# Kernel optimization log

Hardware: AMD Instinct MI355X
Metric: run time of the kernel (lower is better)

Reference implementation:

```python
import jax, jax.numpy as jnp
import numpy as np

EPS = 1e-5
NEG_SLOPE = 0.2


def batchnorm_nodes(x, gamma, beta):
    # BatchNorm2d over channel=node axis; x: [N, T, D], stats over (T, D) per node
    m = x.mean(axis=(1, 2), keepdims=True)
    v = ((x - m) ** 2).mean(axis=(1, 2), keepdims=True)
    return (x - m) * jax.lax.rsqrt(v + EPS) * gamma[:, None, None] + beta[:, None, None]


def gat_relation(h, src, dst, W, al, ar, N):
    # h: [N, T, D]; W: [D, H, dh]; al/ar: [H, dh]
    z = jnp.einsum('ntd,dhe->nthe', h, W)              # [N, T, H, dh]
    el = jnp.einsum('nthe,he->nth', z, al)             # [N, T, H]
    er = jnp.einsum('nthe,he->nth', z, ar)
    e = jax.nn.leaky_relu(el[src] + er[dst], NEG_SLOPE)  # [E, T, H]
    emax = jax.ops.segment_max(e, dst, num_segments=N)   # [N, T, H]
    ex = jnp.exp(e - emax[dst])
    denom = jax.ops.segment_sum(ex, dst, num_segments=N)
    alpha = ex / jnp.maximum(denom[dst], 1e-16)          # segment softmax over in-edges
    msg = alpha[..., None] * z[src]                      # [E, T, H, dh]
    return jax.ops.segment_sum(msg, dst, num_segments=N)  # [N, T, H, dh]


def setup_inputs() -> dict:
    key = jax.random.key(0)
    ks = jax.random.split(key, 12)
    N, T, D, H, E, DFF = 10000, 12, 64, 4, 100000, 128
    dh = D // H
    s = 0.1
    return {
        'x': jax.random.normal(ks[0], (N, T, D), jnp.float32),
        'src1': jax.random.randint(ks[1], (E,), 0, N, jnp.int32),
        'dst1': jax.random.randint(ks[2], (E,), 0, N, jnp.int32),
        'src2': jax.random.randint(ks[3], (E,), 0, N, jnp.int32),
        'dst2': jax.random.randint(ks[4], (E,), 0, N, jnp.int32),
        'W1': jax.random.normal(ks[5], (D, H, dh), jnp.float32) * s,
        'al1': jax.random.normal(ks[6], (H, dh), jnp.float32) * s,
        'ar1': jax.random.normal(ks[7], (H, dh), jnp.float32) * s,
        'W2': jax.random.normal(ks[8], (D, H, dh), jnp.float32) * s,
        'al2': jax.random.normal(ks[9], (H, dh), jnp.float32) * s,
        'ar2': jax.random.normal(ks[10], (H, dh), jnp.float32) * s,
        'bn1_g': jnp.ones((N,), jnp.float32),
        'bn1_b': jnp.zeros((N,), jnp.float32),
        'bn2_g': jnp.ones((N,), jnp.float32),
        'bn2_b': jnp.zeros((N,), jnp.float32),
        'ff_w1': jax.random.normal(ks[11], (D, DFF), jnp.float32) * s,
        'ff_b1': jnp.zeros((DFF,), jnp.float32),
        'ff_w2': jax.random.normal(jax.random.fold_in(key, 99), (DFF, D), jnp.float32) * s,
        'ff_b2': jnp.zeros((D,), jnp.float32),
    }


def reference(x, src1, dst1, src2, dst2, W1, al1, ar1, W2, al2, ar2,
              bn1_g, bn1_b, bn2_g, bn2_b, ff_w1, ff_b1, ff_w2, ff_b2):
    N, T, D = x.shape
    h = batchnorm_nodes(x, bn1_g, bn1_b)
    # HeteroGraphConv: per-relation GAT, sum aggregation
    m = gat_relation(h, src1, dst1, W1, al1, ar1, N) \
      + gat_relation(h, src2, dst2, W2, al2, ar2, N)   # [N, T, H, dh]
    m = m.reshape(N, T, D)
    x2 = x + m                                          # residual (dropout=identity in eval)
    h2 = batchnorm_nodes(x2, bn2_g, bn2_b)
    ff = jax.nn.gelu(h2 @ ff_w1 + ff_b1, approximate=False) @ ff_w2 + ff_b2
    return x2 + ff
```

## Files before the change

kernel.cpp:

```cpp
#include <hip/hip_runtime.h>
#include <math.h>

constexpr int kT = 12;
constexpr float kNeg = 0.2f;
constexpr float kEps = 1e-5f;
constexpr float kLog2e = 1.44269504088896f;

typedef __attribute__((ext_vector_type(8))) short bf16x8;
typedef __attribute__((ext_vector_type(4))) float f32x4;
typedef __attribute__((ext_vector_type(2))) float f32x2;

__device__ __forceinline__ short f2bf(float f) {
  union { float f; unsigned u; } v;
  v.f = f;
  return (short)((v.u + 0x7fffu + ((v.u >> 16) & 1u)) >> 16);
}
__device__ __forceinline__ unsigned pack2(float a, float b) {
  return (unsigned)(unsigned short)f2bf(a) | ((unsigned)(unsigned short)f2bf(b) << 16);
}

__device__ __forceinline__ float wave_reduce_sum(float v) {
#pragma unroll
  for (int o = 32; o > 0; o >>= 1) v += __shfl_xor(v, o);
  return v;
}

template <int CTRL>
__device__ __forceinline__ float qperm(float v) {
  int i = __float_as_int(v);
  return __int_as_float(__builtin_amdgcn_update_dpp(i, i, CTRL, 0xf, 0xf, false));
}

__global__ void prep_kernel(const float* __restrict__ x, const float* __restrict__ g,
                            const float* __restrict__ b, float* __restrict__ scale,
                            float* __restrict__ shift, const float* __restrict__ fw1,
                            const float* __restrict__ fw2, const float* __restrict__ zW1,
                            const float* __restrict__ zW2, const float* __restrict__ al1,
                            const float* __restrict__ ar1, const float* __restrict__ al2,
                            const float* __restrict__ ar2, bf16x8* __restrict__ fw1f,
                            bf16x8* __restrict__ fw2f, bf16x8* __restrict__ zw1f,
                            bf16x8* __restrict__ zw2f, bf16x8* __restrict__ walf,
                            const int* __restrict__ dst1, const int* __restrict__ dst2,
                            int* __restrict__ deg1, int* __restrict__ deg2, int N, int E1,
                            int E2, int nBnBlk) {
  int blk = blockIdx.x;
  int lane = threadIdx.x & 63, wid = threadIdx.x >> 6;
  if (blk < nBnBlk) {
    int n = blk * 4 + wid;
    if (n < N) {
      const float* xr = x + (size_t)n * 768;
      float s = 0.f, s2 = 0.f;
#pragma unroll
      for (int c = 0; c < 3; c++) {
        float4 v = *(const float4*)&xr[c * 256 + lane * 4];
        s += v.x + v.y + v.z + v.w;
        s2 += v.x * v.x + v.y * v.y + v.z * v.z + v.w * v.w;
      }
      s = wave_reduce_sum(s);
      s2 = wave_reduce_sum(s2);
      if (lane == 0) {
        const float inv = 1.f / 768.f;
        float mean = s * inv;
        float var = s2 * inv - mean * mean;
        float sc = rsqrtf(var + kEps) * g[n];
        scale[n] = sc;
        shift[n] = b[n] - mean * sc;
      }
    }
    return;
  }
  blk -= nBnBlk;
  int m = lane & 15, q = lane >> 4;
  if (blk == 0) {
    for (int fi = wid; fi < 16; fi += 4) {
      int mt = fi >> 1, kc = fi & 1;
      int dff = (mt >> 1) * 32 + (m >> 2) * 8 + (mt & 1) * 4 + (m & 3);
      bf16x8 v;
#pragma unroll
      for (int j = 0; j < 8; j++) v[j] = f2bf(fw1[(kc * 32 + q * 8 + j) * 128 + dff]);
      fw1f[fi * 64 + lane] = v;
    }
    return;
  }
  if (blk == 1) {
    for (int fi = wid; fi < 16; fi += 4) {
      int mt2 = fi >> 2, kc2 = fi & 3;
      bf16x8 u;
#pragma unroll
      for (int j = 0; j < 8; j++) u[j] = f2bf(fw2[(kc2 * 32 + q * 8 + j) * 64 + mt2 * 16 + m]);
      fw2f[fi * 64 + lane] = u;
    }
    return;
  }
  if (blk == 2) {
    for (int fi = wid; fi < 8; fi += 4) {
      int mt = fi >> 1, kc = fi & 1;
      bf16x8 v, u;
#pragma unroll
      for (int j = 0; j < 8; j++) {
        int d = kc * 32 + q * 8 + j;
        v[j] = f2bf(zW1[d * 64 + mt * 16 + m]);
        u[j] = f2bf(zW2[d * 64 + mt * 16 + m]);
      }
      zw1f[fi * 64 + lane] = v;
      zw2f[fi * 64 + lane] = u;
    }
    return;
  }
  if (blk == 3) {
    __shared__ float wal[16][64];
    for (int e0 = threadIdx.x; e0 < 1024; e0 += 256) {
      int f = e0 >> 6, d = e0 & 63;
      int h = f & 3;
      const float* av = (f < 4) ? al1 : (f < 8) ? ar1 : (f < 12) ? al2 : ar2;
      const float* W = (f < 8) ? zW1 : zW2;
      float s = 0.f;
#pragma unroll
      for (int e = 0; e < 16; e++) s += W[d * 64 + h * 16 + e] * av[h * 16 + e];
      wal[f][d] = s * kLog2e;
    }
    __syncthreads();
    if (wid == 0) {
#pragma unroll
      for (int kc = 0; kc < 2; kc++) {
        bf16x8 v;
#pragma unroll
        for (int j = 0; j < 8; j++) v[j] = f2bf(wal[m][kc * 32 + q * 8 + j]);
        walf[kc * 64 + lane] = v;
      }
    }
    return;
  }
  int i = (blk - 4) * 256 + threadIdx.x;
  if (i < E1) atomicAdd(&deg1[dst1[i]], 1);
  else if (i < E1 + E2) atomicAdd(&deg2[dst2[i - E1]], 1);
}

__global__ void alloc_kernel(const int* __restrict__ deg1, int* __restrict__ off1,
                             int* __restrict__ ctr1, const int* __restrict__ deg2,
                             int* __restrict__ off2, int* __restrict__ ctr2, int N) {
  int n = blockIdx.x * 256 + threadIdx.x;
  int lane = threadIdx.x & 63;
  int d1 = (n < N) ? deg1[n] : 0;
  int d2 = (n < N) ? deg2[n] : 0;
  int i1 = d1, i2 = d2;
#pragma unroll
  for (int o = 1; o < 64; o <<= 1) {
    int y1 = __shfl_up(i1, o), y2 = __shfl_up(i2, o);
    if (lane >= o) { i1 += y1; i2 += y2; }
  }
  int tot1 = __shfl(i1, 63), tot2 = __shfl(i2, 63);
  int base1 = 0, base2 = 0;
  if (lane == 0) {
    base1 = atomicAdd(ctr1, tot1);
    base2 = atomicAdd(ctr2, tot2);
  }
  base1 = __shfl(base1, 0);
  base2 = __shfl(base2, 0);
  if (n < N) {
    off1[n] = base1 + i1 - d1;
    off2[n] = base2 + i2 - d2;
  }
}

__global__ __launch_bounds__(256, 4) void fillzel_kernel(
    const int* __restrict__ src1, const int* __restrict__ dst1, const int* __restrict__ off1,
    int* __restrict__ cur1, int* __restrict__ scsr1, const int* __restrict__ src2,
    const int* __restrict__ dst2, const int* __restrict__ off2, int* __restrict__ cur2,
    int* __restrict__ scsr2, int E1, int E2, int nZelBlk,
    const float* __restrict__ x, const float* __restrict__ scale,
    const float* __restrict__ shift, const bf16x8* __restrict__ zw1f,
    const bf16x8* __restrict__ zw2f, const bf16x8* __restrict__ walf,
    unsigned short* __restrict__ z1, unsigned short* __restrict__ z2,
    float* __restrict__ el1, float* __restrict__ er1, float* __restrict__ el2,
    float* __restrict__ er2, int NT) {
  if ((int)blockIdx.x >= nZelBlk) {
    int i = ((int)blockIdx.x - nZelBlk) * 256 + threadIdx.x;
    if (i < E1) {
      int d = dst1[i];
      int p = atomicAdd(&cur1[d], 1);
      scsr1[off1[d] + p] = src1[i] * kT;
    } else if (i < E1 + E2) {
      int k = i - E1;
      int d = dst2[k];
      int p = atomicAdd(&cur2[d], 1);
      scsr2[off2[d] + p] = src2[k] * kT;
    }
    return;
  }
  __shared__ bf16x8 sW1[8][64];
  __shared__ bf16x8 sW2[8][64];
  __shared__ bf16x8 sWE[2][64];
  int lane = threadIdx.x & 63, wid = threadIdx.x >> 6;
  int m = lane & 15, q = lane >> 4;
  for (int fi = wid; fi < 8; fi += 4) {
    sW1[fi][lane] = zw1f[fi * 64 + lane];
    sW2[fi][lane] = zw2f[fi * 64 + lane];
  }
  if (wid == 0) {
    sWE[0][lane] = walf[lane];
    sWE[1][lane] = walf[64 + lane];
  }
  __syncthreads();
  int ntile = (NT + 15) / 16;
  int grp = blockIdx.x * 4 + wid;
  if (grp * 2 >= ntile) return;

  bf16x8 hf[2][2];
  float scv[2], shv[2];
  int rowv[2], rowcv[2];
#pragma unroll
  for (int tt = 0; tt < 2; tt++) {
    int tile = grp * 2 + tt;
    int row = tile * 16 + m;
    int rowc = (row < NT) ? row : NT - 1;
    rowv[tt] = row;
    rowcv[tt] = rowc;
    int n = rowc / kT;
    scv[tt] = scale[n];
    shv[tt] = shift[n];
  }
#pragma unroll
  for (int tt = 0; tt < 2; tt++) {
    float sc = scv[tt], sh = shv[tt];
    int rowc = rowcv[tt];
#pragma unroll
    for (int kc = 0; kc < 2; kc++) {
      float4 p0 = *(const float4*)&x[(size_t)rowc * 64 + kc * 32 + q * 8];
      float4 p1 = *(const float4*)&x[(size_t)rowc * 64 + kc * 32 + q * 8 + 4];
      hf[tt][kc][0] = f2bf(fmaf(p0.x, sc, sh));
      hf[tt][kc][1] = f2bf(fmaf(p0.y, sc, sh));
      hf[tt][kc][2] = f2bf(fmaf(p0.z, sc, sh));
      hf[tt][kc][3] = f2bf(fmaf(p0.w, sc, sh));
      hf[tt][kc][4] = f2bf(fmaf(p1.x, sc, sh));
      hf[tt][kc][5] = f2bf(fmaf(p1.y, sc, sh));
      hf[tt][kc][6] = f2bf(fmaf(p1.z, sc, sh));
      hf[tt][kc][7] = f2bf(fmaf(p1.w, sc, sh));
    }
  }
  f32x4 a1[2][4], a2[2][4], ae[2];
#pragma unroll
  for (int tt = 0; tt < 2; tt++) {
#pragma unroll
    for (int mt = 0; mt < 4; mt++) {
      a1[tt][mt] = (f32x4){0.f, 0.f, 0.f, 0.f};
      a2[tt][mt] = (f32x4){0.f, 0.f, 0.f, 0.f};
    }
    ae[tt] = (f32x4){0.f, 0.f, 0.f, 0.f};
  }
#pragma unroll
  for (int kc = 0; kc < 2; kc++) {
#pragma unroll
    for (int mt = 0; mt < 4; mt++) {
#pragma unroll
      for (int tt = 0; tt < 2; tt++) {
        a1[tt][mt] = __builtin_amdgcn_mfma_f32_16x16x32_bf16(sW1[mt * 2 + kc][lane],
                                                             hf[tt][kc], a1[tt][mt], 0, 0, 0);
        a2[tt][mt] = __builtin_amdgcn_mfma_f32_16x16x32_bf16(sW2[mt * 2 + kc][lane],
                                                             hf[tt][kc], a2[tt][mt], 0, 0, 0);
      }
    }
#pragma unroll
    for (int tt = 0; tt < 2; tt++)
      ae[tt] = __builtin_amdgcn_mfma_f32_16x16x32_bf16(sWE[kc][lane], hf[tt][kc], ae[tt], 0,
                                                       0, 0);
  }
#pragma unroll
  for (int tt = 0; tt < 2; tt++) {
    int row = rowv[tt];
    if (row < NT) {
      float* edst = (q == 0) ? el1 : (q == 1) ? er1 : (q == 2) ? el2 : er2;
      *(float4*)&edst[(size_t)row * 4] =
          make_float4(ae[tt][0], ae[tt][1], ae[tt][2], ae[tt][3]);
#pragma unroll
      for (int mt = 0; mt < 4; mt++) {
        uint2 u1 = {pack2(a1[tt][mt][0], a1[tt][mt][1]), pack2(a1[tt][mt][2], a1[tt][mt][3])};
        uint2 u2 = {pack2(a2[tt][mt][0], a2[tt][mt][1]), pack2(a2[tt][mt][2], a2[tt][mt][3])};
        *(uint2*)&z1[(size_t)row * 64 + mt * 16 + 4 * q] = u1;
        *(uint2*)&z2[(size_t)row * 64 + mt * 16 + 4 * q] = u2;
      }
    }
  }
}

struct GBuf {
  uint2 z0, z1, z2, z3;
  float e;
};

__device__ __forceinline__ void pf_group(int sbl, int eb, int t, int zvoff,
                                         const float* __restrict__ elp,
                                         const unsigned short* __restrict__ zp, int qidx,
                                         GBuf& G) {
  int sg = __shfl(sbl, eb + qidx) + t;
  G.e = elp[(size_t)sg * 4];
  int s0 = __builtin_amdgcn_readlane(sbl, eb);
  int s1 = __builtin_amdgcn_readlane(sbl, eb + 1);
  int s2 = __builtin_amdgcn_readlane(sbl, eb + 2);
  int s3 = __builtin_amdgcn_readlane(sbl, eb + 3);
  G.z0 = *(const uint2*)(zp + (size_t)s0 * 64 + zvoff);
  G.z1 = *(const uint2*)(zp + (size_t)s1 * 64 + zvoff);
  G.z2 = *(const uint2*)(zp + (size_t)s2 * 64 + zvoff);
  G.z3 = *(const uint2*)(zp + (size_t)s3 * 64 + zvoff);
}

__device__ __forceinline__ void cg_group(const GBuf& G, float er_h, int rem, int qidx,
                                         float& den, f32x2& n01, f32x2& n23) {
  float ev = G.e + er_h;
  ev = fmaxf(ev, kNeg * ev);
  float w = exp2f(ev);
  w = (qidx < rem) ? w : 0.f;
  den += w;
  float w0 = qperm<0x00>(w);
  float w1 = qperm<0x55>(w);
  float w2 = qperm<0xAA>(w);
  float w3 = qperm<0xFF>(w);
  f32x2 v;
  v = (f32x2){__uint_as_float(G.z0.x << 16), __uint_as_float(G.z0.x & 0xffff0000u)};
  n01 += v * w0;
  v = (f32x2){__uint_as_float(G.z0.y << 16), __uint_as_float(G.z0.y & 0xffff0000u)};
  n23 += v * w0;
  v = (f32x2){__uint_as_float(G.z1.x << 16), __uint_as_float(G.z1.x & 0xffff0000u)};
  n01 += v * w1;
  v = (f32x2){__uint_as_float(G.z1.y << 16), __uint_as_float(G.z1.y & 0xffff0000u)};
  n23 += v * w1;
  v = (f32x2){__uint_as_float(G.z2.x << 16), __uint_as_float(G.z2.x & 0xffff0000u)};
  n01 += v * w2;
  v = (f32x2){__uint_as_float(G.z2.y << 16), __uint_as_float(G.z2.y & 0xffff0000u)};
  n23 += v * w2;
  v = (f32x2){__uint_as_float(G.z3.x << 16), __uint_as_float(G.z3.x & 0xffff0000u)};
  n01 += v * w3;
  v = (f32x2){__uint_as_float(G.z3.y << 16), __uint_as_float(G.z3.y & 0xffff0000u)};
  n23 += v * w3;
}

__device__ __forceinline__ void gat_rel(int b0, int b1, int t, int zvoff,
                                        const int* __restrict__ scsr,
                                        const float* __restrict__ elp, float er_h,
                                        const unsigned short* __restrict__ zp, int lane,
                                        int qidx, f32x2& a01, f32x2& a23) {
  if (b1 <= b0) return;
  float den = 0.f;
  f32x2 n01 = {0.f, 0.f}, n23 = {0.f, 0.f};
  for (int c0 = b0; c0 < b1; c0 += 64) {
    int cnt = b1 - c0;
    if (cnt > 64) cnt = 64;
    int idx = c0 + lane;
    int sbl = scsr[(idx < b1) ? idx : b1 - 1];
    GBuf A, B, C, D;
    pf_group(sbl, 0, t, zvoff, elp, zp, qidx, A);
    if (cnt > 4) pf_group(sbl, 4, t, zvoff, elp, zp, qidx, B);
    if (cnt > 8) pf_group(sbl, 8, t, zvoff, elp, zp, qidx, C);
    int g = 0;
    while (true) {
      if (g + 12 < cnt) pf_group(sbl, g + 12, t, zvoff, elp, zp, qidx, D);
      cg_group(A, er_h, cnt - g, qidx, den, n01, n23);
      g += 4;
      if (g >= cnt) break;
      if (g + 12 < cnt) pf_group(sbl, g + 12, t, zvoff, elp, zp, qidx, A);
      cg_group(B, er_h, cnt - g, qidx, den, n01, n23);
      g += 4;
      if (g >= cnt) break;
      if (g + 12 < cnt) pf_group(sbl, g + 12, t, zvoff, elp, zp, qidx, B);
      cg_group(C, er_h, cnt - g, qidx, den, n01, n23);
      g += 4;
      if (g >= cnt) break;
      if (g + 12 < cnt) pf_group(sbl, g + 12, t, zvoff, elp, zp, qidx, C);
      cg_group(D, er_h, cnt - g, qidx, den, n01, n23);
      g += 4;
      if (g >= cnt) break;
    }
  }
  den += qperm<0xB1>(den);
  den += qperm<0x4E>(den);
  float inv = 1.f / den;
  a01 += n01 * inv;
  a23 += n23 * inv;
}

__global__ __launch_bounds__(256) void agg_kernel(
    const float* __restrict__ x, const int* __restrict__ scsr1,
    const int* __restrict__ off1, const int* __restrict__ deg1,
    const float* __restrict__ el1, const float* __restrict__ er1,
    const unsigned short* __restrict__ z1, const int* __restrict__ scsr2,
    const int* __restrict__ off2, const int* __restrict__ deg2,
    const float* __restrict__ el2, const float* __restrict__ er2,
    const unsigned short* __restrict__ z2, float* __restrict__ x2,
    float* __restrict__ bn2s, float* __restrict__ bn2q, int N) {
  int wid = threadIdx.x >> 6, lane = threadIdx.x & 63;
  int w = blockIdx.x * 4 + wid;
  if (w >= N * 3) return;
  int n = w / 3;
  int t0 = (w - n * 3) * 4;
  int tl = lane >> 4, cg = lane & 15;
  int t = t0 + tl;
  int row = n * kT + t;
  int h = cg >> 2;
  int qidx = lane & 3;
  int zvoff = t * 64 + cg * 4;
  f32x2 a01 = {0.f, 0.f}, a23 = {0.f, 0.f};
  int b0a = off1[n], b1a = b0a + deg1[n];
  int b0b = off2[n], b1b = b0b + deg2[n];
  gat_rel(b0a, b1a, t, zvoff, scsr1, el1 + h, er1[(size_t)row * 4 + h], z1, lane, qidx, a01,
          a23);
  gat_rel(b0b, b1b, t, zvoff, scsr2, el2 + h, er2[(size_t)row * 4 + h], z2, lane, qidx, a01,
          a23);

  size_t base = (size_t)row * 64 + cg * 4;
  float4 xr = *(const float4*)&x[base];
  float4 o;
  o.x = xr.x + a01.x;
  o.y = xr.y + a01.y;
  o.z = xr.z + a23.x;
  o.w = xr.w + a23.y;
  *(float4*)&x2[base] = o;
  float s1 = o.x + o.y + o.z + o.w;
  float s2 = o.x * o.x + o.y * o.y + o.z * o.z + o.w * o.w;
  s1 = wave_reduce_sum(s1);
  s2 = wave_reduce_sum(s2);
  if (lane == 0) {
    atomicAdd(&bn2s[n], s1);
    atomicAdd(&bn2q[n], s2);
  }
}

__global__ __launch_bounds__(256, 4) void ff_kernel(
    const float* __restrict__ x2, const float* __restrict__ bn2s,
    const float* __restrict__ bn2q, const float* __restrict__ bng,
    const float* __restrict__ bnb, const bf16x8* __restrict__ w1f,
    const bf16x8* __restrict__ w2f, const float* __restrict__ b1,
    const float* __restrict__ b2, float* __restrict__ out, int NT) {
  __shared__ bf16x8 sW1[16][64];
  __shared__ bf16x8 sW2[16][64];
  __shared__ float sB1[128];
  __shared__ float sB2[64];
  int lane = threadIdx.x & 63, wid = threadIdx.x >> 6;
  int m = lane & 15, q = lane >> 4;
  {
    int fi0 = wid * 4;
#pragma unroll
    for (int k = 0; k < 4; k++) {
      sW1[fi0 + k][lane] = w1f[(fi0 + k) * 64 + lane];
      sW2[fi0 + k][lane] = w2f[(fi0 + k) * 64 + lane];
    }
    if (threadIdx.x < 128) sB1[threadIdx.x] = b1[threadIdx.x];
    if (threadIdx.x < 64) sB2[threadIdx.x] = b2[threadIdx.x];
  }
  __syncthreads();

  const float inv = 1.f / 768.f;
  int grp = blockIdx.x * 4 + wid;
  int ngrp = (NT + 31) / 32;
  if (grp >= ngrp) return;

  bf16x8 hf[2][2];
  f32x4 acc[2][8];
#pragma unroll
  for (int tt = 0; tt < 2; tt++) {
    int row = grp * 32 + tt * 16 + m;
    int rowc = (row < NT) ? row : NT - 1;
    int n = rowc / kT;
    float mean = bn2s[n] * inv;
    float var = bn2q[n] * inv - mean * mean;
    float sc = rsqrtf(var + kEps) * bng[n];
    float sh = bnb[n] - mean * sc;
#pragma unroll
    for (int kc = 0; kc < 2; kc++) {
      const float4 p0 = *(const float4*)&x2[(size_t)rowc * 64 + kc * 32 + q * 8];
      const float4 p1 = *(const float4*)&x2[(size_t)rowc * 64 + kc * 32 + q * 8 + 4];
      hf[tt][kc][0] = f2bf(fmaf(p0.x, sc, sh));
      hf[tt][kc][1] = f2bf(fmaf(p0.y, sc, sh));
      hf[tt][kc][2] = f2bf(fmaf(p0.z, sc, sh));
      hf[tt][kc][3] = f2bf(fmaf(p0.w, sc, sh));
      hf[tt][kc][4] = f2bf(fmaf(p1.x, sc, sh));
      hf[tt][kc][5] = f2bf(fmaf(p1.y, sc, sh));
      hf[tt][kc][6] = f2bf(fmaf(p1.z, sc, sh));
      hf[tt][kc][7] = f2bf(fmaf(p1.w, sc, sh));
    }
#pragma unroll
    for (int mt = 0; mt < 8; mt++) acc[tt][mt] = (f32x4){0.f, 0.f, 0.f, 0.f};
  }
#pragma unroll
  for (int kc = 0; kc < 2; kc++)
#pragma unroll
    for (int mt = 0; mt < 8; mt++)
#pragma unroll
      for (int tt = 0; tt < 2; tt++)
        acc[tt][mt] = __builtin_amdgcn_mfma_f32_16x16x32_bf16(sW1[mt * 2 + kc][lane],
                                                              hf[tt][kc], acc[tt][mt], 0, 0, 0);

  f32x4 acc2[2][4];
#pragma unroll
  for (int tt = 0; tt < 2; tt++)
#pragma unroll
    for (int mt = 0; mt < 4; mt++) acc2[tt][mt] = (f32x4){0.f, 0.f, 0.f, 0.f};
#pragma unroll
  for (int kc = 0; kc < 4; kc++) {
    float4 bb0 = *(const float4*)&sB1[kc * 32 + q * 8];
    float4 bb1 = *(const float4*)&sB1[kc * 32 + q * 8 + 4];
    bf16x8 bf[2];
#pragma unroll
    for (int tt = 0; tt < 2; tt++) {
      float u;
      u = acc[tt][2 * kc][0] + bb0.x; bf[tt][0] = f2bf(0.5f * u * (1.f + erff(u * 0.70710678118654752f)));
      u = acc[tt][2 * kc][1] + bb0.y; bf[tt][1] = f2bf(0.5f * u * (1.f + erff(u * 0.70710678118654752f)));
      u = acc[tt][2 * kc][2] + bb0.z; bf[tt][2] = f2bf(0.5f * u * (1.f + erff(u * 0.70710678118654752f)));
      u = acc[tt][2 * kc][3] + bb0.w; bf[tt][3] = f2bf(0.5f * u * (1.f + erff(u * 0.70710678118654752f)));
      u = acc[tt][2 * kc + 1][0] + bb1.x; bf[tt][4] = f2bf(0.5f * u * (1.f + erff(u * 0.70710678118654752f)));
      u = acc[tt][2 * kc + 1][1] + bb1.y; bf[tt][5] = f2bf(0.5f * u * (1.f + erff(u * 0.70710678118654752f)));
      u = acc[tt][2 * kc + 1][2] + bb1.z; bf[tt][6] = f2bf(0.5f * u * (1.f + erff(u * 0.70710678118654752f)));
      u = acc[tt][2 * kc + 1][3] + bb1.w; bf[tt][7] = f2bf(0.5f * u * (1.f + erff(u * 0.70710678118654752f)));
    }
#pragma unroll
    for (int mt = 0; mt < 4; mt++)
#pragma unroll
      for (int tt = 0; tt < 2; tt++)
        acc2[tt][mt] = __builtin_amdgcn_mfma_f32_16x16x32_bf16(sW2[mt * 4 + kc][lane], bf[tt],
                                                               acc2[tt][mt], 0, 0, 0);
  }

#pragma unroll
  for (int tt = 0; tt < 2; tt++) {
    int row = grp * 32 + tt * 16 + m;
    if (row < NT) {
#pragma unroll
      for (int mt = 0; mt < 4; mt++) {
        size_t base = (size_t)row * 64 + mt * 16 + 4 * q;
        float4 xr = *(const float4*)&x2[base];
        float4 bb = *(const float4*)&sB2[mt * 16 + 4 * q];
        float4 o;
        o.x = acc2[tt][mt][0] + bb.x + xr.x;
        o.y = acc2[tt][mt][1] + bb.y + xr.y;
        o.z = acc2[tt][mt][2] + bb.z + xr.z;
        o.w = acc2[tt][mt][3] + bb.w + xr.w;
        *(float4*)&out[base] = o;
      }
    }
  }
}

extern "C" void kernel_launch(void* const* d_in, const int* in_sizes, int n_in,
                              void* d_out, int out_size, void* d_ws, size_t ws_size,
                              hipStream_t stream) {
  const float* x = (const float*)d_in[0];
  const int* src1 = (const int*)d_in[1];
  const int* dst1 = (const int*)d_in[2];
  const int* src2 = (const int*)d_in[3];
  const int* dst2 = (const int*)d_in[4];
  const float* W1 = (const float*)d_in[5];
  const float* al1 = (const float*)d_in[6];
  const float* ar1 = (const float*)d_in[7];
  const float* W2 = (const float*)d_in[8];
  const float* al2 = (const float*)d_in[9];
  const float* ar2 = (const float*)d_in[10];
  const float* g1 = (const float*)d_in[11];
  const float* b1 = (const float*)d_in[12];
  const float* g2 = (const float*)d_in[13];
  const float* b2 = (const float*)d_in[14];
  const float* fw1 = (const float*)d_in[15];
  const float* fb1 = (const float*)d_in[16];
  const float* fw2 = (const float*)d_in[17];
  const float* fb2 = (const float*)d_in[18];

  const int N = in_sizes[11];
  const int E1 = in_sizes[1];
  const int E2 = in_sizes[3];
  const int NT = N * kT;

  char* p = (char*)d_ws;
  auto alloc = [&](size_t bytes) -> char* {
    char* r = p;
    p += (bytes + 255) & ~(size_t)255;
    return r;
  };
  unsigned short* z1 = (unsigned short*)alloc((size_t)NT * 64 * 2);
  unsigned short* z2 = (unsigned short*)alloc((size_t)NT * 64 * 2);
  float* el1 = (float*)alloc((size_t)NT * 4 * 4);
  float* er1 = (float*)alloc((size_t)NT * 4 * 4);
  float* el2 = (float*)alloc((size_t)NT * 4 * 4);
  float* er2 = (float*)alloc((size_t)NT * 4 * 4);
  float* x2 = (float*)alloc((size_t)NT * 64 * 4);
  float* sc1 = (float*)alloc((size_t)N * 4);
  float* sh1 = (float*)alloc((size_t)N * 4);
  int* off1 = (int*)alloc((size_t)(N + 1) * 4);
  int* off2 = (int*)alloc((size_t)(N + 1) * 4);
  int* scsr1 = (int*)alloc((size_t)E1 * 4);
  int* scsr2 = (int*)alloc((size_t)E2 * 4);
  bf16x8* fw1f = (bf16x8*)alloc(16 * 64 * 16);
  bf16x8* fw2f = (bf16x8*)alloc(16 * 64 * 16);
  bf16x8* zw1f = (bf16x8*)alloc(8 * 64 * 16);
  bf16x8* zw2f = (bf16x8*)alloc(8 * 64 * 16);
  bf16x8* walf = (bf16x8*)alloc(2 * 64 * 16);
  char* zero_base = p;
  int* deg1 = (int*)alloc((size_t)N * 4);
  int* cur1 = (int*)alloc((size_t)N * 4);
  int* deg2 = (int*)alloc((size_t)N * 4);
  int* cur2 = (int*)alloc((size_t)N * 4);
  float* bn2s = (float*)alloc((size_t)N * 4);
  float* bn2q = (float*)alloc((size_t)N * 4);
  int* ctrs = (int*)alloc(2 * 4);
  size_t zero_bytes = (size_t)(p - zero_base);
  hipMemsetAsync(zero_base, 0, zero_bytes, stream);

  const int nBnBlk = (N + 3) / 4;
  const int degBlk = (E1 + E2 + 255) / 256;
  prep_kernel<<<nBnBlk + 4 + degBlk, 256, 0, stream>>>(
      x, g1, b1, sc1, sh1, fw1, fw2, W1, W2, al1, ar1, al2, ar2, fw1f, fw2f, zw1f, zw2f, walf,
      dst1, dst2, deg1, deg2, N, E1, E2, nBnBlk);
  alloc_kernel<<<(N + 255) / 256, 256, 0, stream>>>(deg1, off1, &ctrs[0], deg2, off2,
                                                    &ctrs[1], N);
  const int ntile = (NT + 15) / 16;
  const int nZelBlk = (ntile / 2 + 3) / 4;
  fillzel_kernel<<<nZelBlk + degBlk, 256, 0, stream>>>(
      src1, dst1, off1, cur1, scsr1, src2, dst2, off2, cur2, scsr2, E1, E2, nZelBlk, x, sc1,
      sh1, zw1f, zw2f, walf, z1, z2, el1, er1, el2, er2, NT);
  agg_kernel<<<(N * 3 + 3) / 4, 256, 0, stream>>>(x, scsr1, off1, deg1, el1, er1, z1, scsr2,
                                                  off2, deg2, el2, er2, z2, x2, bn2s, bn2q, N);
  ff_kernel<<<((NT + 31) / 32 + 3) / 4, 256, 0, stream>>>(x2, bn2s, bn2q, g2, b2, fw1f, fw2f,
                                                          fb1, fb2, (float*)d_out, NT);
}
```

Measured before the change: 234.6 us.

## Fuse GAT aggregation, second batchnorm and feed-forward into one kernel

Merges the aggregation kernel and the FF kernel so each block owns four nodes. The residual sum x2 stays in shared memory, and the per-node batchnorm stats are computed in-wave instead of with global atomics. This removes the x2 global round trip, the bn2 stat buffers and atomics, and one kernel launch. In exchange each wave now processes all 12 time steps of a node serially, the grid is a third as large, only 3 of 4 waves do the MFMA stage, and the extra shared memory and launch bound of 3 may reduce occupancy.

```diff
diff --git a/kernel.cpp b/kernel.cpp
--- a/kernel.cpp
+++ b/kernel.cpp
@@ -378,62 +378,23 @@
   a23 += n23 * inv;
 }
 
-__global__ __launch_bounds__(256) void agg_kernel(
+__global__ __launch_bounds__(256, 3) void aggff_kernel(
     const float* __restrict__ x, const int* __restrict__ scsr1,
     const int* __restrict__ off1, const int* __restrict__ deg1,
     const float* __restrict__ el1, const float* __restrict__ er1,
     const unsigned short* __restrict__ z1, const int* __restrict__ scsr2,
     const int* __restrict__ off2, const int* __restrict__ deg2,
     const float* __restrict__ el2, const float* __restrict__ er2,
-    const unsigned short* __restrict__ z2, float* __restrict__ x2,
-    float* __restrict__ bn2s, float* __restrict__ bn2q, int N) {
-  int wid = threadIdx.x >> 6, lane = threadIdx.x & 63;
-  int w = blockIdx.x * 4 + wid;
-  if (w >= N * 3) return;
-  int n = w / 3;
-  int t0 = (w - n * 3) * 4;
-  int tl = lane >> 4, cg = lane & 15;
-  int t = t0 + tl;
-  int row = n * kT + t;
-  int h = cg >> 2;
-  int qidx = lane & 3;
-  int zvoff = t * 64 + cg * 4;
-  f32x2 a01 = {0.f, 0.f}, a23 = {0.f, 0.f};
-  int b0a = off1[n], b1a = b0a + deg1[n];
-  int b0b = off2[n], b1b = b0b + deg2[n];
-  gat_rel(b0a, b1a, t, zvoff, scsr1, el1 + h, er1[(size_t)row * 4 + h], z1, lane, qidx, a01,
-          a23);
-  gat_rel(b0b, b1b, t, zvoff, scsr2, el2 + h, er2[(size_t)row * 4 + h], z2, lane, qidx, a01,
-          a23);
-
-  size_t base = (size_t)row * 64 + cg * 4;
-  float4 xr = *(const float4*)&x[base];
-  float4 o;
-  o.x = xr.x + a01.x;
-  o.y = xr.y + a01.y;
-  o.z = xr.z + a23.x;
-  o.w = xr.w + a23.y;
-  *(float4*)&x2[base] = o;
-  float s1 = o.x + o.y + o.z + o.w;
-  float s2 = o.x * o.x + o.y * o.y + o.z * o.z + o.w * o.w;
-  s1 = wave_reduce_sum(s1);
-  s2 = wave_reduce_sum(s2);
-  if (lane == 0) {
-    atomicAdd(&bn2s[n], s1);
-    atomicAdd(&bn2q[n], s2);
-  }
-}
-
-__global__ __launch_bounds__(256, 4) void ff_kernel(
-    const float* __restrict__ x2, const float* __restrict__ bn2s,
-    const float* __restrict__ bn2q, const float* __restrict__ bng,
+    const unsigned short* __restrict__ z2, const float* __restrict__ bng,
     const float* __restrict__ bnb, const bf16x8* __restrict__ w1f,
     const bf16x8* __restrict__ w2f, const float* __restrict__ b1,
-    const float* __restrict__ b2, float* __restrict__ out, int NT) {
+    const float* __restrict__ b2, float* __restrict__ out, int N, int NT) {
   __shared__ bf16x8 sW1[16][64];
   __shared__ bf16x8 sW2[16][64];
   __shared__ float sB1[128];
   __shared__ float sB2[64];
+  __shared__ float x2s[48][68];
+  __shared__ float nsc[4], nsh[4];
   int lane = threadIdx.x & 63, wid = threadIdx.x >> 6;
   int m = lane & 15, q = lane >> 4;
   {
@@ -446,95 +407,117 @@
     if (threadIdx.x < 128) sB1[threadIdx.x] = b1[threadIdx.x];
     if (threadIdx.x < 64) sB2[threadIdx.x] = b2[threadIdx.x];
   }
+
+  int n = blockIdx.x * 4 + wid;
+  int tl = lane >> 4, cg = lane & 15;
+  int h = cg >> 2;
+  int qidx = lane & 3;
+  if (n < N) {
+    int b0a = off1[n], b1a = b0a + deg1[n];
+    int b0b = off2[n], b1b = b0b + deg2[n];
+    float s1acc = 0.f, s2acc = 0.f;
+#pragma unroll
+    for (int p = 0; p < 3; p++) {
+      int t = p * 4 + tl;
+      int row = n * kT + t;
+      int zvoff = t * 64 + cg * 4;
+      f32x2 a01 = {0.f, 0.f}, a23 = {0.f, 0.f};
+      gat_rel(b0a, b1a, t, zvoff, scsr1, el1 + h, er1[(size_t)row * 4 + h], z1, lane, qidx,
+              a01, a23);
+      gat_rel(b0b, b1b, t, zvoff, scsr2, el2 + h, er2[(size_t)row * 4 + h], z2, lane, qidx,
+              a01, a23);
+      size_t base = (size_t)row * 64 + cg * 4;
+      float4 xr = *(const float4*)&x[base];
+      float4 o;
+      o.x = xr.x + a01.x;
+      o.y = xr.y + a01.y;
+      o.z = xr.z + a23.x;
+      o.w = xr.w + a23.y;
+      *(float4*)&x2s[wid * 12 + t][cg * 4] = o;
+      s1acc += o.x + o.y + o.z + o.w;
+      s2acc += o.x * o.x + o.y * o.y + o.z * o.z + o.w * o.w;
+    }
+    float s1 = wave_reduce_sum(s1acc);
+    float s2 = wave_reduce_sum(s2acc);
+    if (lane == 0) {
+      const float inv = 1.f / 768.f;
+      float mean = s1 * inv;
+      float var = s2 * inv - mean * mean;
+      float sc = rsqrtf(var + kEps) * bng[n];
+      nsc[wid] = sc;
+      nsh[wid] = bnb[n] - mean * sc;
+    }
+  } else if (lane == 0) {
+    nsc[wid] = 0.f;
+    nsh[wid] = 0.f;
+  }
   __syncthreads();
 
-  const float inv = 1.f / 768.f;
-  int grp = blockIdx.x * 4 + wid;
-  int ngrp = (NT + 31) / 32;
-  if (grp >= ngrp) return;
-
-  bf16x8 hf[2][2];
-  f32x4 acc[2][8];
-#pragma unroll
-  for (int tt = 0; tt < 2; tt++) {
-    int row = grp * 32 + tt * 16 + m;
-    int rowc = (row < NT) ? row : NT - 1;
-    int n = rowc / kT;
-    float mean = bn2s[n] * inv;
-    float var = bn2q[n] * inv - mean * mean;
-    float sc = rsqrtf(var + kEps) * bng[n];
-    float sh = bnb[n] - mean * sc;
-#pragma unroll
-    for (int kc = 0; kc < 2; kc++) {
-      const float4 p0 = *(const float4*)&x2[(size_t)rowc * 64 + kc * 32 + q * 8];
-      const float4 p1 = *(const float4*)&x2[(size_t)rowc * 64 + kc * 32 + q * 8 + 4];
-      hf[tt][kc][0] = f2bf(fmaf(p0.x, sc, sh));
-      hf[tt][kc][1] = f2bf(fmaf(p0.y, sc, sh));
-      hf[tt][kc][2] = f2bf(fmaf(p0.z, sc, sh));
-      hf[tt][kc][3] = f2bf(fmaf(p0.w, sc, sh));
-      hf[tt][kc][4] = f2bf(fmaf(p1.x, sc, sh));
-      hf[tt][kc][5] = f2bf(fmaf(p1.y, sc, sh));
-      hf[tt][kc][6] = f2bf(fmaf(p1.z, sc, sh));
-      hf[tt][kc][7] = f2bf(fmaf(p1.w, sc, sh));
-    }
-#pragma unroll
-    for (int mt = 0; mt < 8; mt++) acc[tt][mt] = (f32x4){0.f, 0.f, 0.f, 0.f};
-  }
+  if (wid >= 3) return;
+  int lrow = wid * 16 + m;
+  int grow = blockIdx.x * 48 + lrow;
+  float sc = nsc[lrow / kT], sh = nsh[lrow / kT];
+
+  bf16x8 hf[2];
+#pragma unroll
+  for (int kc = 0; kc < 2; kc++) {
+    const float4 p0 = *(const float4*)&x2s[lrow][kc * 32 + q * 8];
+    const float4 p1 = *(const float4*)&x2s[lrow][kc * 32 + q * 8 + 4];
+    hf[kc][0] = f2bf(fmaf(p0.x, sc, sh));
+    hf[kc][1] = f2bf(fmaf(p0.y, sc, sh));
+    hf[kc][2] = f2bf(fmaf(p0.z, sc, sh));
+    hf[kc][3] = f2bf(fmaf(p0.w, sc, sh));
+    hf[kc][4] = f2bf(fmaf(p1.x, sc, sh));
+    hf[kc][5] = f2bf(fmaf(p1.y, sc, sh));
+    hf[kc][6] = f2bf(fmaf(p1.z, sc, sh));
+    hf[kc][7] = f2bf(fmaf(p1.w, sc, sh));
+  }
+
+  f32x4 acc[8];
+#pragma unroll
+  for (int mt = 0; mt < 8; mt++) acc[mt] = (f32x4){0.f, 0.f, 0.f, 0.f};
 #pragma unroll
   for (int kc = 0; kc < 2; kc++)
 #pragma unroll
     for (int mt = 0; mt < 8; mt++)
-#pragma unroll
-      for (int tt = 0; tt < 2; tt++)
-        acc[tt][mt] = __builtin_amdgcn_mfma_f32_16x16x32_bf16(sW1[mt * 2 + kc][lane],
-                                                              hf[tt][kc], acc[tt][mt], 0, 0, 0);
-
-  f32x4 acc2[2][4];
-#pragma unroll
-  for (int tt = 0; tt < 2; tt++)
-#pragma unroll
-    for (int mt = 0; mt < 4; mt++) acc2[tt][mt] = (f32x4){0.f, 0.f, 0.f, 0.f};
+      acc[mt] = __builtin_amdgcn_mfma_f32_16x16x32_bf16(sW1[mt * 2 + kc][lane], hf[kc],
+                                                        acc[mt], 0, 0, 0);
+
+  f32x4 acc2[4];
+#pragma unroll
+  for (int mt = 0; mt < 4; mt++) acc2[mt] = (f32x4){0.f, 0.f, 0.f, 0.f};
 #pragma unroll
   for (int kc = 0; kc < 4; kc++) {
     float4 bb0 = *(const float4*)&sB1[kc * 32 + q * 8];
     float4 bb1 = *(const float4*)&sB1[kc * 32 + q * 8 + 4];
-    bf16x8 bf[2];
-#pragma unroll
-    for (int tt = 0; tt < 2; tt++) {
-      float u;
-      u = acc[tt][2 * kc][0] + bb0.x; bf[tt][0] = f2bf(0.5f * u * (1.f + erff(u * 0.70710678118654752f)));
-      u = acc[tt][2 * kc][1] + bb0.y; bf[tt][1] = f2bf(0.5f * u * (1.f + erff(u * 0.70710678118654752f)));
-      u = acc[tt][2 * kc][2] + bb0.z; bf[tt][2] = f2bf(0.5f * u * (1.f + erff(u * 0.70710678118654752f)));
-      u = acc[tt][2 * kc][3] + bb0.w; bf[tt][3] = f2bf(0.5f * u * (1.f + erff(u * 0.70710678118654752f)));
-      u = acc[tt][2 * kc + 1][0] + bb1.x; bf[tt][4] = f2bf(0.5f * u * (1.f + erff(u * 0.70710678118654752f)));
-      u = acc[tt][2 * kc + 1][1] + bb1.y; bf[tt][5] = f2bf(0.5f * u * (1.f + erff(u * 0.70710678118654752f)));
-      u = acc[tt][2 * kc + 1][2] + bb1.z; bf[tt][6] = f2bf(0.5f * u * (1.f + erff(u * 0.70710678118654752f)));
-      u = acc[tt][2 * kc + 1][3] + bb1.w; bf[tt][7] = f2bf(0.5f * u * (1.f + erff(u * 0.70710678118654752f)));
-    }
+    bf16x8 bf;
+    float u;
+    u = acc[2 * kc][0] + bb0.x; bf[0] = f2bf(0.5f * u * (1.f + erff(u * 0.70710678118654752f)));
+    u = acc[2 * kc][1] + bb0.y; bf[1] = f2bf(0.5f * u * (1.f + erff(u * 0.70710678118654752f)));
+    u = acc[2 * kc][2] + bb0.z; bf[2] = f2bf(0.5f * u * (1.f + erff(u * 0.70710678118654752f)));
+    u = acc[2 * kc][3] + bb0.w; bf[3] = f2bf(0.5f * u * (1.f + erff(u * 0.70710678118654752f)));
+    u = acc[2 * kc + 1][0] + bb1.x; bf[4] = f2bf(0.5f * u * (1.f + erff(u * 0.70710678118654752f)));
+    u = acc[2 * kc + 1][1] + bb1.y; bf[5] = f2bf(0.5f * u * (1.f + erff(u * 0.70710678118654752f)));
+    u = acc[2 * kc + 1][2] + bb1.z; bf[6] = f2bf(0.5f * u * (1.f + erff(u * 0.70710678118654752f)));
+    u = acc[2 * kc + 1][3] + bb1.w; bf[7] = f2bf(0.5f * u * (1.f + erff(u * 0.70710678118654752f)));
 #pragma unroll
     for (int mt = 0; mt < 4; mt++)
-#pragma unroll
-      for (int tt = 0; tt < 2; tt++)
-        acc2[tt][mt] = __builtin_amdgcn_mfma_f32_16x16x32_bf16(sW2[mt * 4 + kc][lane], bf[tt],
-                                                               acc2[tt][mt], 0, 0, 0);
-  }
-
-#pragma unroll
-  for (int tt = 0; tt < 2; tt++) {
-    int row = grp * 32 + tt * 16 + m;
-    if (row < NT) {
-#pragma unroll
-      for (int mt = 0; mt < 4; mt++) {
-        size_t base = (size_t)row * 64 + mt * 16 + 4 * q;
-        float4 xr = *(const float4*)&x2[base];
-        float4 bb = *(const float4*)&sB2[mt * 16 + 4 * q];
-        float4 o;
-        o.x = acc2[tt][mt][0] + bb.x + xr.x;
-        o.y = acc2[tt][mt][1] + bb.y + xr.y;
-        o.z = acc2[tt][mt][2] + bb.z + xr.z;
-        o.w = acc2[tt][mt][3] + bb.w + xr.w;
-        *(float4*)&out[base] = o;
-      }
+      acc2[mt] = __builtin_amdgcn_mfma_f32_16x16x32_bf16(sW2[mt * 4 + kc][lane], bf, acc2[mt],
+                                                         0, 0, 0);
+  }
+
+  if (grow < NT) {
+#pragma unroll
+    for (int mt = 0; mt < 4; mt++) {
+      size_t base = (size_t)grow * 64 + mt * 16 + 4 * q;
+      float4 xr = *(const float4*)&x2s[lrow][mt * 16 + 4 * q];
+      float4 bb = *(const float4*)&sB2[mt * 16 + 4 * q];
+      float4 o;
+      o.x = acc2[mt][0] + bb.x + xr.x;
+      o.y = acc2[mt][1] + bb.y + xr.y;
+      o.z = acc2[mt][2] + bb.z + xr.z;
+      o.w = acc2[mt][3] + bb.w + xr.w;
+      *(float4*)&out[base] = o;
     }
   }
 }
@@ -579,7 +562,6 @@
   float* er1 = (float*)alloc((size_t)NT * 4 * 4);
   float* el2 = (float*)alloc((size_t)NT * 4 * 4);
   float* er2 = (float*)alloc((size_t)NT * 4 * 4);
-  float* x2 = (float*)alloc((size_t)NT * 64 * 4);
   float* sc1 = (float*)alloc((size_t)N * 4);
   float* sh1 = (float*)alloc((size_t)N * 4);
   int* off1 = (int*)alloc((size_t)(N + 1) * 4);
@@ -596,8 +578,6 @@
   int* cur1 = (int*)alloc((size_t)N * 4);
   int* deg2 = (int*)alloc((size_t)N * 4);
   int* cur2 = (int*)alloc((size_t)N * 4);
-  float* bn2s = (float*)alloc((size_t)N * 4);
-  float* bn2q = (float*)alloc((size_t)N * 4);
   int* ctrs = (int*)alloc(2 * 4);
   size_t zero_bytes = (size_t)(p - zero_base);
   hipMemsetAsync(zero_base, 0, zero_bytes, stream);
@@ -614,8 +594,7 @@
   fillzel_kernel<<<nZelBlk + degBlk, 256, 0, stream>>>(
       src1, dst1, off1, cur1, scsr1, src2, dst2, off2, cur2, scsr2, E1, E2, nZelBlk, x, sc1,
       sh1, zw1f, zw2f, walf, z1, z2, el1, er1, el2, er2, NT);
-  agg_kernel<<<(N * 3 + 3) / 4, 256, 0, stream>>>(x, scsr1, off1, deg1, el1, er1, z1, scsr2,
-                                                  off2, deg2, el2, er2, z2, x2, bn2s, bn2q, N);
-  ff_kernel<<<((NT + 31) / 32 + 3) / 4, 256, 0, stream>>>(x2, bn2s, bn2q, g2, b2, fw1f, fw2f,
-                                                          fb1, fb2, (float*)d_out, NT);
-}
+  aggff_kernel<<<(N + 3) / 4, 256, 0, stream>>>(x, scsr1, off1, deg1, el1, er1, z1, scsr2,
+                                                off2, deg2, el2, er2, z2, g2, b2, fw1f, fw2f,
+                                                fb1, fb2, (float*)d_out, N, NT);
+}
```

Measured after the change: 233.7 us. No clear change (-0.4%).
